# Performance work log

Hardware: AMD Instinct MI355X
Metric: run time of the kernel (lower is better)

The kernel has to match this reference:

```python
import jax, jax.numpy as jnp
import numpy as np

MUL = 256            # multiplicity of each irrep block
S = MUL              # scalar (0e) block width
V = MUL * 3          # vector (1e) block width
D = S + V            # total feature width = 1024
N = 32768            # number of nodes
INV3 = 1.0 / np.sqrt(3.0)   # w3j(1,1,0) and w3j(0,1,1) coefficient
INV6 = 1.0 / np.sqrt(6.0)   # w3j(1,1,1) (Levi-Civita) coefficient
A0 = np.sqrt(1.0 / 5.0)     # path weight for 0e outputs: sqrt(dim_out / n_paths) = sqrt(1/5)
A1 = np.sqrt(3.0 / 5.0)     # path weight for 1e outputs: sqrt(3/5)


def _split(x):
    # x: [N, D] -> scalars [N, MUL], vectors [N, MUL, 3]
    return x[:, :S], x[:, S:].reshape(x.shape[0], MUL, 3)


def norm_gate(x, w1, b1, w2, b2):
    # NormGate: gates = MLP([scalars, |vectors|]); out = [gates_s, vectors * gates_v]
    s, v = _split(x)
    nv = jnp.sqrt(jnp.sum(v * v, axis=-1) + 1e-12)           # [N, MUL] per-irrep norms
    f0 = jnp.concatenate([s, nv], axis=-1)                    # [N, 2*MUL]
    g = jax.nn.silu(f0 @ w1 + b1) @ w2 + b2                   # [N, 2*MUL]
    gated = v * g[:, S:, None]                                # ElementwiseTensorProduct with 0e gates
    return jnp.concatenate([g[:, :S], gated.reshape(-1, V)], axis=-1)


def irrep_linear(x, w0, b0, w1):
    # e3nn o3.Linear: per-l multiplicity mixing with 1/sqrt(fan_in) normalization; bias only on 0e
    s, v = _split(x)
    so = s @ (w0 / np.sqrt(MUL)) + b0
    vo = jnp.einsum('nui,uw->nwi', v, w1 / np.sqrt(MUL))
    return jnp.concatenate([so, vo.reshape(-1, V)], axis=-1)


def tensor_product(x1, x2, w):
    # 'uuu' CG tensor product, 5 instructions: (0,0)->0, (0,1)->1, (1,0)->1, (1,1)->0, (1,1)->1
    # w: [5, MUL] per-path per-u learned weights
    s1, v1 = _split(x1)
    s2, v2 = _split(x2)
    out0 = A0 * (w[0] * s1 * s2 + w[3] * INV3 * jnp.sum(v1 * v2, axis=-1))   # [N, MUL]
    out1 = A1 * (INV3 * (w[1] * s1)[:, :, None] * v2
                 + INV3 * (w[2] * s2)[:, :, None] * v1
                 + INV6 * w[4][None, :, None] * jnp.cross(v1, v2))           # [N, MUL, 3]
    return jnp.concatenate([out0, out1.reshape(-1, V)], axis=-1)


def setup_inputs() -> dict:
    key = jax.random.key(0)
    ks = jax.random.split(key, 32)
    d = {}
    d['x'] = jax.random.normal(ks[0], (N, D), dtype=jnp.float32)
    d['old_fii'] = jax.random.normal(ks[1], (N, D), dtype=jnp.float32)
    i = 2
    for pre in ('ng1', 'ng2', 'ngo'):
        d[pre + '_w1'] = jax.random.normal(ks[i], (2 * MUL, 2 * MUL), dtype=jnp.float32) / np.sqrt(2 * MUL); i += 1
        d[pre + '_b1'] = jax.random.normal(ks[i], (2 * MUL,), dtype=jnp.float32) * 0.01; i += 1
        d[pre + '_w2'] = jax.random.normal(ks[i], (2 * MUL, 2 * MUL), dtype=jnp.float32) / np.sqrt(2 * MUL); i += 1
        d[pre + '_b2'] = jax.random.normal(ks[i], (2 * MUL,), dtype=jnp.float32) * 0.01; i += 1
    for pre in ('lin1', 'lin2', 'lin3'):
        d[pre + '_w0'] = jax.random.normal(ks[i], (MUL, MUL), dtype=jnp.float32); i += 1
        d[pre + '_b0'] = jax.random.normal(ks[i], (MUL,), dtype=jnp.float32) * 0.01; i += 1
        d[pre + '_w1'] = jax.random.normal(ks[i], (MUL, MUL), dtype=jnp.float32); i += 1
    d['tp_w'] = jax.random.normal(ks[i], (5, MUL), dtype=jnp.float32)
    return d


def reference(x, old_fii,
              ng1_w1, ng1_b1, ng1_w2, ng1_b2,
              ng2_w1, ng2_b1, ng2_w2, ng2_b2,
              ngo_w1, ngo_b1, ngo_w2, ngo_b2,
              lin1_w0, lin1_b0, lin1_w1,
              lin2_w0, lin2_b0, lin2_w1,
              lin3_w0, lin3_b0, lin3_w1,
              tp_w):
    xl = irrep_linear(norm_gate(x, ng1_w1, ng1_b1, ng1_w2, ng1_b2), lin1_w0, lin1_b0, lin1_w1)
    xr = irrep_linear(norm_gate(x, ng2_w1, ng2_b1, ng2_w2, ng2_b2), lin2_w0, lin2_b0, lin2_w1)
    t = tensor_product(xl, xr, tp_w) + x        # resnet (dims match)
    t = irrep_linear(norm_gate(t, ngo_w1, ngo_b1, ngo_w2, ngo_b2), lin3_w0, lin3_b0, lin3_w1)
    return old_fii + t
```

## Files before the change

### kernel.cpp

```cpp
#include <hip/hip_runtime.h>
#include <stdint.h>
#include <math.h>

typedef unsigned short u16;
typedef __attribute__((ext_vector_type(8))) short short8;
typedef __attribute__((ext_vector_type(4))) float f32x4;

#define A0C 0.44721359549995793f
#define A1C 0.77459666924148340f
#define INV3C 0.57735026918962584f
#define INV6C 0.40824829046386302f

__device__ __forceinline__ float bf2f(u16 u) {
    unsigned v = ((unsigned)u) << 16; float f; __builtin_memcpy(&f, &v, 4); return f;
}
__device__ __forceinline__ u16 f2bf(float f) {
    unsigned u; __builtin_memcpy(&u, &f, 4);
    u += 0x7fffu + ((u >> 16) & 1u);
    return (u16)(u >> 16);
}

__device__ __forceinline__ void gload_lds16(const void* g, void* l) {
    __builtin_amdgcn_global_load_lds((const __attribute__((address_space(1))) unsigned*)g,
                                     (__attribute__((address_space(3))) unsigned*)l, 16, 0, 0);
}

union S8 { short8 v; u16 h[8]; };

struct WDesc { const float* s; u16* d; int n; float sc; };
struct WArgs { WDesc w[12]; };

__global__ void cvt_weights(WArgs args) {
    WDesc wd = args.w[blockIdx.z];
    int n = wd.n;
    int x0 = blockIdx.x * 32, y0 = blockIdx.y * 32;
    if (x0 >= n || y0 >= n) return;
    __shared__ float tile[32][33];
    int tx = threadIdx.x, ty = threadIdx.y;
#pragma unroll
    for (int j = 0; j < 4; j++)
        tile[ty + 8 * j][tx] = wd.s[(size_t)(y0 + ty + 8 * j) * n + x0 + tx];
    __syncthreads();
#pragma unroll
    for (int j = 0; j < 4; j++)
        wd.d[(size_t)(x0 + ty + 8 * j) * n + y0 + tx] = f2bf(tile[tx][ty + 8 * j] * wd.sc);
}

struct BDesc { const float* s; float* d; int n; };
struct BArgs { BDesc b[9]; };
__global__ void pack_bias(BArgs a) {
    BDesc b = a.b[blockIdx.x];
    for (int i = threadIdx.x; i < b.n; i += 256) b.d[i] = b.s[i];
}

__global__ void prep_f0(const float* __restrict__ x, u16* __restrict__ f0,
                        u16* __restrict__ xv, long ps) {
    int t = blockIdx.x * 256 + threadIdx.x;
    long n = t >> 5;
    int u0 = (t & 31) * 8;
    const float* xr = x + (size_t)n * 1024;
    float4 s0 = *(const float4*)(xr + u0);
    float4 s1 = *(const float4*)(xr + u0 + 4);
    float vv[24];
#pragma unroll
    for (int i = 0; i < 6; i++) {
        float4 w = *(const float4*)(xr + 256 + 3 * u0 + 4 * i);
        vv[4 * i] = w.x; vv[4 * i + 1] = w.y; vv[4 * i + 2] = w.z; vv[4 * i + 3] = w.w;
    }
    float sc[8] = { s0.x, s0.y, s0.z, s0.w, s1.x, s1.y, s1.z, s1.w };
    S8 fs, fn, px, py, pz;
#pragma unroll
    for (int j = 0; j < 8; j++) {
        float a = vv[3 * j], b = vv[3 * j + 1], c = vv[3 * j + 2];
        float nv = sqrtf(a * a + b * b + c * c + 1e-12f);
        fs.h[j] = f2bf(sc[j]);
        fn.h[j] = f2bf(nv);
        px.h[j] = f2bf(a); py.h[j] = f2bf(b); pz.h[j] = f2bf(c);
    }
    size_t o = (size_t)n * 256 + u0;
    *(short8*)(f0 + (size_t)n * 512 + u0) = fs.v;
    *(short8*)(f0 + (size_t)n * 512 + 256 + u0) = fn.v;
    *(short8*)(xv + o) = px.v;
    *(short8*)(xv + ps + o) = py.v;
    *(short8*)(xv + 2 * ps + o) = pz.v;
}

__global__ __launch_bounds__(512, 2)
void gemm256(const u16* __restrict__ Ap, int lda, long az,
             const u16* __restrict__ xsrc,
             const u16* __restrict__ gp, int gld, long gz,
             const u16* __restrict__ Bt, long bz, long bw,
             const float* __restrict__ bias, int bsz,
             u16* __restrict__ C, int ldc, long czs, long czp,
             int K, long nc, int mode, int act, int nshift)
{
    extern __shared__ __align__(16) u16 sm[];
    u16* As = sm;
    u16* Bs = sm + 32768;

    const int tid = threadIdx.x;
    const int lane = tid & 63;
    const int wid = tid >> 6;
    const int wr = wid >> 2, wc = wid & 3;
    const int lr = lane & 15, hk = lane >> 4;

    int nwg = gridDim.x;
    int lid = blockIdx.x;
    int wg;
    if ((nwg & 7) == 0) { int q = nwg >> 3; wg = (lid & 7) * q + (lid >> 3); }
    else wg = lid;
    const long row0 = (long)(wg >> nshift) * 256;
    const int n0 = (wg & ((1 << nshift) - 1)) * 256;
    const int zi = blockIdx.y;

    long p = 0, rr0 = row0;
    if (mode == 2) { p = row0 / nc; rr0 = row0 - p * nc; }

    const u16* Bz = Bt + (size_t)zi * bz + ((mode == 2 && p > 0) ? bw : 0);
    const long cbase = (mode == 2) ? (zi * czs + p * czp + rr0 * ldc)
                                   : (zi * czs + row0 * ldc);

    f32x4 acc[8][4];
#pragma unroll
    for (int m = 0; m < 8; m++)
#pragma unroll
        for (int n = 0; n < 4; n++) acc[m][n] = (f32x4){0.f, 0.f, 0.f, 0.f};

    auto stageB = [&](int buf, int kt) {
#pragma unroll
        for (int it = 0; it < 4; ++it) {
            int idx = it * 512 + tid;
            int r = idx >> 3, s = idx & 7;
            const u16* g = Bz + (size_t)(n0 + r) * K + kt + ((s ^ (r & 7)) * 8);
            u16* l = Bs + buf * 16384 + (size_t)(it * 512 + (tid & 0x1C0)) * 8;
            gload_lds16(g, l);
        }
    };
    auto stageA0 = [&](int buf, int kt) {
#pragma unroll
        for (int it = 0; it < 4; ++it) {
            int idx = it * 512 + tid;
            int r = idx >> 3, s = idx & 7;
            const u16* g = Ap + (size_t)zi * az + (rr0 + r) * (size_t)lda + kt + ((s ^ (r & 7)) * 8);
            u16* l = As + buf * 16384 + (size_t)(it * 512 + (tid & 0x1C0)) * 8;
            gload_lds16(g, l);
        }
    };
    auto stageA2 = [&](int buf, int kt) {
#pragma unroll
        for (int it = 0; it < 4; ++it) {
            int idx = it * 512 + tid;
            int r = idx >> 3, s = idx & 7;
            int u = kt + s * 8;
            S8 gg, tu, pk;
            gg.v = *(const short8*)(gp + (size_t)zi * gz + (rr0 + r) * (size_t)gld + 256 + u);
            tu.v = *(const short8*)(xsrc + (size_t)(row0 - nc + r) * 256 + u);
#pragma unroll
            for (int j = 0; j < 8; j++) pk.h[j] = f2bf(bf2f(tu.h[j]) * bf2f(gg.h[j]));
            *(short8*)&As[buf * 16384 + ((size_t)r * 8 + (s ^ (r & 7))) * 8] = pk.v;
        }
    };

    auto compute = [&](int buf) {
        const int ao = buf * 16384, bo = buf * 16384;
#pragma unroll
        for (int kk = 0; kk < 2; ++kk) {
            short8 b[4];
#pragma unroll
            for (int n = 0; n < 4; n++) {
                int cb = wc * 64 + n * 16 + lr;
                int sl = (kk * 4 + hk) ^ (cb & 7);
                b[n] = *(const short8*)&Bs[bo + (size_t)cb * 64 + sl * 8];
            }
#pragma unroll
            for (int m = 0; m < 8; m++) {
                int ra = wr * 128 + m * 16 + lr;
                int sl = (kk * 4 + hk) ^ (ra & 7);
                short8 a = *(const short8*)&As[ao + (size_t)ra * 64 + sl * 8];
#pragma unroll
                for (int n = 0; n < 4; n++)
                    acc[m][n] = __builtin_amdgcn_mfma_f32_16x16x32_bf16(b[n], a, acc[m][n], 0, 0, 0);
            }
        }
    };

    const bool a_direct = (mode == 0) || (p == 0);
    const int nt = K >> 6;
    int buf = 0;

    if (a_direct) {
        stageB(0, 0);
        stageA0(0, 0);
        for (int t = 0; t < nt; ++t) {
            if (t + 1 < nt) {
                int kt = (t + 1) << 6;
                stageB(buf ^ 1, kt);
                stageA0(buf ^ 1, kt);
                asm volatile("s_waitcnt vmcnt(8)" ::: "memory");
            } else {
                asm volatile("s_waitcnt vmcnt(0)" ::: "memory");
            }
            __builtin_amdgcn_s_barrier();
            __builtin_amdgcn_sched_barrier(0);
            compute(buf);
            __builtin_amdgcn_s_barrier();
            buf ^= 1;
        }
    } else {
        stageB(0, 0);
        stageA2(0, 0);
        __syncthreads();
        for (int t = 0; t < nt; ++t) {
            if (t + 1 < nt) {
                int kt = (t + 1) << 6;
                stageB(buf ^ 1, kt);
                stageA2(buf ^ 1, kt);
            }
            compute(buf);
            __syncthreads();
            buf ^= 1;
        }
    }

    const bool use_bias = bias && (mode == 0 || p == 0);
#pragma unroll
    for (int m = 0; m < 8; m++) {
        long rit = wr * 128 + m * 16 + lr;
        u16* crow = C + cbase + rit * (size_t)ldc;
#pragma unroll
        for (int n = 0; n < 4; n++) {
            int col = n0 + wc * 64 + n * 16 + hk * 4;
            float4 bb = use_bias ? *(const float4*)&bias[(size_t)zi * bsz + col]
                                 : (float4){0.f, 0.f, 0.f, 0.f};
            float v0 = acc[m][n][0] + bb.x;
            float v1 = acc[m][n][1] + bb.y;
            float v2 = acc[m][n][2] + bb.z;
            float v3 = acc[m][n][3] + bb.w;
            if (act) {
                v0 = v0 * (1.0f / (1.0f + __expf(-v0)));
                v1 = v1 * (1.0f / (1.0f + __expf(-v1)));
                v2 = v2 * (1.0f / (1.0f + __expf(-v2)));
                v3 = v3 * (1.0f / (1.0f + __expf(-v3)));
            }
            uint2 st;
            st.x = (unsigned)f2bf(v0) | ((unsigned)f2bf(v1) << 16);
            st.y = (unsigned)f2bf(v2) | ((unsigned)f2bf(v3) << 16);
            *(uint2*)(crow + col) = st;
        }
    }
}

__global__ void tp_res(const u16* __restrict__ xl, const u16* xr_,
                       const float* __restrict__ tpw, const u16* __restrict__ xv,
                       u16* f0, u16* tv, long ps)
{
    int t = blockIdx.x * 256 + threadIdx.x;
    long n = t >> 5;
    int u0 = (t & 31) * 8;
    size_t o = (size_t)n * 256 + u0;

    S8 S1, AX, AY, AZ, S2, BX, BY, BZ, XS, RX, RY, RZ;
    S1.v = *(const short8*)(xl + o);
    AX.v = *(const short8*)(xl + ps + o);
    AY.v = *(const short8*)(xl + 2 * ps + o);
    AZ.v = *(const short8*)(xl + 3 * ps + o);
    S2.v = *(const short8*)(xr_ + o);
    BX.v = *(const short8*)(xr_ + ps + o);
    BY.v = *(const short8*)(xr_ + 2 * ps + o);
    BZ.v = *(const short8*)(xr_ + 3 * ps + o);
    XS.v = *(const short8*)(f0 + (size_t)n * 512 + u0);
    RX.v = *(const short8*)(xv + o);
    RY.v = *(const short8*)(xv + ps + o);
    RZ.v = *(const short8*)(xv + 2 * ps + o);

    float W[5][8];
#pragma unroll
    for (int q = 0; q < 5; q++) {
        float4 a = *(const float4*)(tpw + q * 256 + u0);
        float4 b = *(const float4*)(tpw + q * 256 + u0 + 4);
        W[q][0] = a.x; W[q][1] = a.y; W[q][2] = a.z; W[q][3] = a.w;
        W[q][4] = b.x; W[q][5] = b.y; W[q][6] = b.z; W[q][7] = b.w;
    }

    S8 O0, NV, TX, TY, TZ;
#pragma unroll
    for (int j = 0; j < 8; j++) {
        float s1 = bf2f(S1.h[j]), a1x = bf2f(AX.h[j]), a1y = bf2f(AY.h[j]), a1z = bf2f(AZ.h[j]);
        float s2 = bf2f(S2.h[j]), b1x = bf2f(BX.h[j]), b1y = bf2f(BY.h[j]), b1z = bf2f(BZ.h[j]);
        float dot = a1x * b1x + a1y * b1y + a1z * b1z;
        float cx = a1y * b1z - a1z * b1y;
        float cy = a1z * b1x - a1x * b1z;
        float cz = a1x * b1y - a1y * b1x;
        float out0 = A0C * (W[0][j] * s1 * s2 + W[3][j] * INV3C * dot) + bf2f(XS.h[j]);
        float ox = A1C * (INV3C * (W[1][j] * s1 * b1x + W[2][j] * s2 * a1x) + INV6C * W[4][j] * cx) + bf2f(RX.h[j]);
        float oy = A1C * (INV3C * (W[1][j] * s1 * b1y + W[2][j] * s2 * a1y) + INV6C * W[4][j] * cy) + bf2f(RY.h[j]);
        float oz = A1C * (INV3C * (W[1][j] * s1 * b1z + W[2][j] * s2 * a1z) + INV6C * W[4][j] * cz) + bf2f(RZ.h[j]);
        float nv = sqrtf(ox * ox + oy * oy + oz * oz + 1e-12f);
        O0.h[j] = f2bf(out0);
        NV.h[j] = f2bf(nv);
        TX.h[j] = f2bf(ox); TY.h[j] = f2bf(oy); TZ.h[j] = f2bf(oz);
    }
    *(short8*)(f0 + (size_t)n * 512 + u0) = O0.v;
    *(short8*)(f0 + (size_t)n * 512 + 256 + u0) = NV.v;
    *(short8*)(tv + o) = TX.v;
    *(short8*)(tv + ps + o) = TY.v;
    *(short8*)(tv + 2 * ps + o) = TZ.v;
}

__global__ void repack(const u16* __restrict__ outp, const float* __restrict__ old,
                       float* __restrict__ out, long ps)
{
    int t = blockIdx.x * 256 + threadIdx.x;
    long n = t >> 5;
    int u0 = (t & 31) * 8;
    size_t o = (size_t)n * 256 + u0;

    S8 S, VX, VY, VZ;
    S.v  = *(const short8*)(outp + o);
    VX.v = *(const short8*)(outp + ps + o);
    VY.v = *(const short8*)(outp + 2 * ps + o);
    VZ.v = *(const short8*)(outp + 3 * ps + o);

    const float* oldr = old + (size_t)n * 1024;
    float* outr = out + (size_t)n * 1024;

#pragma unroll
    for (int i = 0; i < 2; i++) {
        float4 ov = *(const float4*)(oldr + u0 + 4 * i);
        float4 r;
        r.x = ov.x + bf2f(S.h[4 * i]);
        r.y = ov.y + bf2f(S.h[4 * i + 1]);
        r.z = ov.z + bf2f(S.h[4 * i + 2]);
        r.w = ov.w + bf2f(S.h[4 * i + 3]);
        *(float4*)(outr + u0 + 4 * i) = r;
    }
    float vv[24];
#pragma unroll
    for (int j = 0; j < 8; j++) {
        vv[3 * j] = bf2f(VX.h[j]);
        vv[3 * j + 1] = bf2f(VY.h[j]);
        vv[3 * j + 2] = bf2f(VZ.h[j]);
    }
#pragma unroll
    for (int i = 0; i < 6; i++) {
        float4 ov = *(const float4*)(oldr + 256 + 3 * u0 + 4 * i);
        float4 r;
        r.x = ov.x + vv[4 * i];
        r.y = ov.y + vv[4 * i + 1];
        r.z = ov.z + vv[4 * i + 2];
        r.w = ov.w + vv[4 * i + 3];
        *(float4*)(outr + 256 + 3 * u0 + 4 * i) = r;
    }
}

enum {
    OFF_ng12w1 = 0,
    OFF_ng1w2  = 524288,
    OFF_ngow1  = 1048576,
    OFF_ngow2  = 1310720,
    OFF_l12w0  = 1572864,
    OFF_l12w1  = 1703936,
    OFF_l3w0   = 1835008,
    OFF_l3w1   = 1900544
};
#define BIAS_BYTE_OFF 3932160
enum { BOFF_mlp1 = 0, BOFF_mlp2 = 1024, BOFF_ngo1 = 2048, BOFF_ngo2 = 2560,
       BOFF_l12 = 3072, BOFF_l3 = 3584 };

extern "C" void kernel_launch(void* const* d_in, const int* in_sizes, int n_in,
                              void* d_out, int out_size, void* d_ws, size_t ws_size,
                              hipStream_t stream) {
    const float* x      = (const float*)d_in[0];
    const float* oldf   = (const float*)d_in[1];
    const float* ng1_w1 = (const float*)d_in[2];
    const float* ng1_b1 = (const float*)d_in[3];
    const float* ng1_w2 = (const float*)d_in[4];
    const float* ng1_b2 = (const float*)d_in[5];
    const float* ng2_w1 = (const float*)d_in[6];
    const float* ng2_b1 = (const float*)d_in[7];
    const float* ng2_w2 = (const float*)d_in[8];
    const float* ng2_b2 = (const float*)d_in[9];
    const float* ngo_w1 = (const float*)d_in[10];
    const float* ngo_b1 = (const float*)d_in[11];
    const float* ngo_w2 = (const float*)d_in[12];
    const float* ngo_b2 = (const float*)d_in[13];
    const float* l1_w0  = (const float*)d_in[14];
    const float* l1_b0  = (const float*)d_in[15];
    const float* l1_w1  = (const float*)d_in[16];
    const float* l2_w0  = (const float*)d_in[17];
    const float* l2_b0  = (const float*)d_in[18];
    const float* l2_w1  = (const float*)d_in[19];
    const float* l3_w0  = (const float*)d_in[20];
    const float* l3_b0  = (const float*)d_in[21];
    const float* l3_w1  = (const float*)d_in[22];
    const float* tpw    = (const float*)d_in[23];

    u16* wts = (u16*)d_ws;
    char* wsb = (char*)d_ws;
    float* biasf = (float*)(wsb + BIAS_BYTE_OFF);

    WArgs wa;
    wa.w[0]  = { ng1_w1, wts + OFF_ng12w1,          512, 1.0f };
    wa.w[1]  = { ng2_w1, wts + OFF_ng12w1 + 262144, 512, 1.0f };
    wa.w[2]  = { ng1_w2, wts + OFF_ng1w2,           512, 1.0f };
    wa.w[3]  = { ng2_w2, wts + OFF_ng1w2 + 262144,  512, 1.0f };
    wa.w[4]  = { ngo_w1, wts + OFF_ngow1,           512, 1.0f };
    wa.w[5]  = { ngo_w2, wts + OFF_ngow2,           512, 1.0f };
    wa.w[6]  = { l1_w0, wts + OFF_l12w0,            256, 0.0625f };
    wa.w[7]  = { l2_w0, wts + OFF_l12w0 + 65536,    256, 0.0625f };
    wa.w[8]  = { l1_w1, wts + OFF_l12w1,            256, 0.0625f };
    wa.w[9]  = { l2_w1, wts + OFF_l12w1 + 65536,    256, 0.0625f };
    wa.w[10] = { l3_w0, wts + OFF_l3w0,             256, 0.0625f };
    wa.w[11] = { l3_w1, wts + OFF_l3w1,             256, 0.0625f };
    cvt_weights<<<dim3(16, 16, 12), dim3(32, 8), 0, stream>>>(wa);

    BArgs ba;
    ba.b[0] = { ng1_b1, biasf + BOFF_mlp1,       512 };
    ba.b[1] = { ng2_b1, biasf + BOFF_mlp1 + 512, 512 };
    ba.b[2] = { ng1_b2, biasf + BOFF_mlp2,       512 };
    ba.b[3] = { ng2_b2, biasf + BOFF_mlp2 + 512, 512 };
    ba.b[4] = { ngo_b1, biasf + BOFF_ngo1,       512 };
    ba.b[5] = { ngo_b2, biasf + BOFF_ngo2,       512 };
    ba.b[6] = { l1_b0, biasf + BOFF_l12,         256 };
    ba.b[7] = { l2_b0, biasf + BOFF_l12 + 256,   256 };
    ba.b[8] = { l3_b0, biasf + BOFF_l3,          256 };
    pack_bias<<<9, 256, 0, stream>>>(ba);

    long Nn = (long)in_sizes[0] / 1024;

    int c = 1;
    while (c < 256 &&
           (unsigned long long)(4ULL << 20) + (unsigned long long)(Nn / c) * 10752ULL > (unsigned long long)ws_size)
        c <<= 1;
    long Nc = Nn / c;

    u16* F0 = (u16*)(wsb + (4 << 20));
    u16* H  = F0 + (size_t)Nc * 512;
    u16* G  = H + (size_t)Nc * 1024;
    u16* XV = G + (size_t)Nc * 1024;
    u16* XL = XV + (size_t)Nc * 768;
    long ps = Nc * 256;
    u16* XR = XL + 4 * ps;
    u16* TV = XR + ps;
    u16* OUTP = XL;

    dim3 blk(512);
    const size_t SMEM = 131072;
    int mt = (int)(Nc / 256);
    int eb = (int)(Nc / 8);

    for (int ch = 0; ch < c; ++ch) {
        const float* xk  = x + (size_t)ch * Nc * 1024;
        const float* ok  = oldf + (size_t)ch * Nc * 1024;
        float* outk = (float*)d_out + (size_t)ch * Nc * 1024;

        prep_f0<<<eb, 256, 0, stream>>>(xk, F0, XV, ps);

        gemm256<<<dim3(mt * 4, 1), blk, SMEM, stream>>>(F0, 512, 0, nullptr, nullptr, 0, 0,
            wts + OFF_ng12w1, 0, 0, biasf + BOFF_mlp1, 0, H, 1024, 0, 0, 512, Nc, 0, 1, 2);
        gemm256<<<dim3(mt * 2, 2), blk, SMEM, stream>>>(H, 1024, 512, nullptr, nullptr, 0, 0,
            wts + OFF_ng1w2, 262144, 0, biasf + BOFF_mlp2, 512, G, 1024, 512, 0, 512, Nc, 0, 0, 1);
        gemm256<<<dim3(mt * 4, 2), blk, SMEM, stream>>>(G, 1024, 512, XV, G, 1024, 512,
            wts + OFF_l12w0, 65536, 131072, biasf + BOFF_l12, 256, XL, 256, 4 * ps, ps, 256, Nc, 2, 0, 0);

        tp_res<<<eb, 256, 0, stream>>>(XL, XR, tpw, XV, F0, TV, ps);

        gemm256<<<dim3(mt * 2, 1), blk, SMEM, stream>>>(F0, 512, 0, nullptr, nullptr, 0, 0,
            wts + OFF_ngow1, 0, 0, biasf + BOFF_ngo1, 0, H, 512, 0, 0, 512, Nc, 0, 1, 1);
        gemm256<<<dim3(mt * 2, 1), blk, SMEM, stream>>>(H, 512, 0, nullptr, nullptr, 0, 0,
            wts + OFF_ngow2, 0, 0, biasf + BOFF_ngo2, 0, G, 512, 0, 0, 512, Nc, 0, 0, 1);
        gemm256<<<dim3(mt * 4, 1), blk, SMEM, stream>>>(G, 512, 0, TV, G, 512, 0,
            wts + OFF_l3w0, 0, 65536, biasf + BOFF_l3, 0, OUTP, 256, 0, ps, 256, Nc, 2, 0, 0);

        repack<<<eb, 256, 0, stream>>>(OUTP, ok, outk, ps);
    }
}
```

Measured before the change: 504.6 us.

## Fuse the two norm-gate MLP GEMMs into one kernel keeping hidden activations in LDS

Adds a mlp_fused kernel that computes silu(F0@W1+b1) for a 64-row tile, keeps the 64x512 hidden tile in shared memory, then multiplies by W2 and writes the gates directly. This replaces two gemm256 launches per MLP, so the hidden matrix H no longer makes a round trip through global memory. The cost is much smaller row tiles (64 rows instead of 256), so weights are re-streamed more often. It also uses 144 KB of LDS per block, which may limit occupancy to one workgroup per CU.

```diff
diff --git a/kernel.cpp b/kernel.cpp
--- a/kernel.cpp
+++ b/kernel.cpp
@@ -83,6 +83,179 @@
     *(short8*)(xv + o) = px.v;
     *(short8*)(xv + ps + o) = py.v;
     *(short8*)(xv + 2 * ps + o) = pz.v;
+}
+
+__global__ __launch_bounds__(512, 2)
+void mlp_fused(const u16* __restrict__ F0, int ldf,
+               const u16* __restrict__ W1, long w1zs,
+               const u16* __restrict__ W2, long w2zs,
+               const float* __restrict__ B1, int b1zs,
+               const float* __restrict__ B2, int b2zs,
+               u16* __restrict__ G, int ldg, int gzoff,
+               long nc)
+{
+    extern __shared__ __align__(16) u16 sm[];
+    u16* Hs = sm;
+    u16* St = sm + 32768;
+
+    const int tid = threadIdx.x;
+    const int lane = tid & 63;
+    const int wid = tid >> 6;
+    const int lr = lane & 15, hk = lane >> 4;
+
+    int nwg = gridDim.x;
+    int lid = blockIdx.x;
+    int wg;
+    if ((nwg & 7) == 0) { int q = nwg >> 3; wg = (lid & 7) * q + (lid >> 3); }
+    else wg = lid;
+    const long rows0 = (long)wg * 64;
+    const int z = blockIdx.y;
+
+    const u16* W1z = W1 + (size_t)z * w1zs;
+    const u16* W2z = W2 + (size_t)z * w2zs;
+    const float* b1 = B1 + (size_t)z * b1zs;
+    const float* b2 = B2 + (size_t)z * b2zs;
+
+    f32x4 acc[4][2];
+
+    auto stageB = [&](const u16* Bh, int buf, int kt) {
+        u16* Bd = St + buf * 20480;
+#pragma unroll
+        for (int it = 0; it < 4; ++it) {
+            int idx = it * 512 + tid;
+            int r = idx >> 3, s = idx & 7;
+            gload_lds16(Bh + (size_t)r * 512 + kt + ((s ^ (r & 7)) * 8),
+                        Bd + (size_t)(it * 512 + (tid & 0x1C0)) * 8);
+        }
+    };
+    auto stageA = [&](int buf, int kt) {
+        u16* Ad = St + buf * 20480 + 16384;
+        int r = tid >> 3, s = tid & 7;
+        gload_lds16(F0 + (rows0 + r) * (size_t)ldf + kt + ((s ^ (r & 7)) * 8),
+                    Ad + (size_t)(tid & 0x1C0) * 8);
+    };
+
+    auto comp1 = [&](int buf) {
+        const u16* Bd = St + buf * 20480;
+        const u16* Ad = Bd + 16384;
+#pragma unroll
+        for (int kk = 0; kk < 2; ++kk) {
+            short8 b[2];
+#pragma unroll
+            for (int n = 0; n < 2; n++) {
+                int cb = wid * 32 + n * 16 + lr;
+                int sl = (kk * 4 + hk) ^ (cb & 7);
+                b[n] = *(const short8*)&Bd[(size_t)cb * 64 + sl * 8];
+            }
+#pragma unroll
+            for (int m = 0; m < 4; m++) {
+                int ra = m * 16 + lr;
+                int sl = (kk * 4 + hk) ^ (ra & 7);
+                short8 a = *(const short8*)&Ad[(size_t)ra * 64 + sl * 8];
+#pragma unroll
+                for (int n = 0; n < 2; n++)
+                    acc[m][n] = __builtin_amdgcn_mfma_f32_16x16x32_bf16(b[n], a, acc[m][n], 0, 0, 0);
+            }
+        }
+    };
+    auto comp2 = [&](int buf, int kt) {
+        const u16* Bd = St + buf * 20480;
+#pragma unroll
+        for (int kk = 0; kk < 2; ++kk) {
+            short8 b[2];
+#pragma unroll
+            for (int n = 0; n < 2; n++) {
+                int cb = wid * 32 + n * 16 + lr;
+                int sl = (kk * 4 + hk) ^ (cb & 7);
+                b[n] = *(const short8*)&Bd[(size_t)cb * 64 + sl * 8];
+            }
+#pragma unroll
+            for (int m = 0; m < 4; m++) {
+                int ra = m * 16 + lr;
+                int slot = ((kt >> 3) + kk * 4 + hk) ^ (ra & 7);
+                short8 a = *(const short8*)&Hs[(size_t)ra * 512 + slot * 8];
+#pragma unroll
+                for (int n = 0; n < 2; n++)
+                    acc[m][n] = __builtin_amdgcn_mfma_f32_16x16x32_bf16(b[n], a, acc[m][n], 0, 0, 0);
+            }
+        }
+    };
+
+    for (int nh = 0; nh < 2; ++nh) {
+        const u16* Bh = W1z + (size_t)nh * 256 * 512;
+#pragma unroll
+        for (int m = 0; m < 4; m++)
+#pragma unroll
+            for (int n = 0; n < 2; n++) acc[m][n] = (f32x4){0.f, 0.f, 0.f, 0.f};
+        stageB(Bh, 0, 0);
+        stageA(0, 0);
+        __syncthreads();
+        int buf = 0;
+        for (int t = 0; t < 8; ++t) {
+            if (t + 1 < 8) { stageB(Bh, buf ^ 1, (t + 1) << 6); stageA(buf ^ 1, (t + 1) << 6); }
+            comp1(buf);
+            __syncthreads();
+            buf ^= 1;
+        }
+#pragma unroll
+        for (int m = 0; m < 4; m++) {
+            int row = m * 16 + lr;
+#pragma unroll
+            for (int n = 0; n < 2; n++) {
+                int col = nh * 256 + wid * 32 + n * 16 + hk * 4;
+                float4 bb = *(const float4*)&b1[col];
+                float v0 = acc[m][n][0] + bb.x;
+                float v1 = acc[m][n][1] + bb.y;
+                float v2 = acc[m][n][2] + bb.z;
+                float v3 = acc[m][n][3] + bb.w;
+                v0 = v0 * (1.0f / (1.0f + __expf(-v0)));
+                v1 = v1 * (1.0f / (1.0f + __expf(-v1)));
+                v2 = v2 * (1.0f / (1.0f + __expf(-v2)));
+                v3 = v3 * (1.0f / (1.0f + __expf(-v3)));
+                uint2 st;
+                st.x = (unsigned)f2bf(v0) | ((unsigned)f2bf(v1) << 16);
+                st.y = (unsigned)f2bf(v2) | ((unsigned)f2bf(v3) << 16);
+                int slot = (col >> 3) ^ (row & 7);
+                *(uint2*)&Hs[(size_t)row * 512 + slot * 8 + (col & 7)] = st;
+            }
+        }
+        __syncthreads();
+    }
+
+    for (int nh = 0; nh < 2; ++nh) {
+        const u16* Bh = W2z + (size_t)nh * 256 * 512;
+#pragma unroll
+        for (int m = 0; m < 4; m++)
+#pragma unroll
+            for (int n = 0; n < 2; n++) acc[m][n] = (f32x4){0.f, 0.f, 0.f, 0.f};
+        stageB(Bh, 0, 0);
+        __syncthreads();
+        int buf = 0;
+        for (int t = 0; t < 8; ++t) {
+            if (t + 1 < 8) stageB(Bh, buf ^ 1, (t + 1) << 6);
+            comp2(buf, t << 6);
+            __syncthreads();
+            buf ^= 1;
+        }
+#pragma unroll
+        for (int m = 0; m < 4; m++) {
+            int row = m * 16 + lr;
+            u16* grow = G + (rows0 + row) * (size_t)ldg + (size_t)z * gzoff;
+#pragma unroll
+            for (int n = 0; n < 2; n++) {
+                int col = nh * 256 + wid * 32 + n * 16 + hk * 4;
+                float4 bb = *(const float4*)&b2[col];
+                float v0 = acc[m][n][0] + bb.x;
+                float v1 = acc[m][n][1] + bb.y;
+                float v2 = acc[m][n][2] + bb.z;
+                float v3 = acc[m][n][3] + bb.w;
+                uint2 st;
+                st.x = (unsigned)f2bf(v0) | ((unsigned)f2bf(v1) << 16);
+                st.y = (unsigned)f2bf(v2) | ((unsigned)f2bf(v3) << 16);
+                *(uint2*)(grow + col) = st;
+            }
+        }
+    }
 }
 
 __global__ __launch_bounds__(512, 2)
@@ -446,7 +619,9 @@
 
     dim3 blk(512);
     const size_t SMEM = 131072;
+    const size_t SMEM_MLP = 147456;
     int mt = (int)(Nc / 256);
+    int fb = (int)(Nc / 64);
     int eb = (int)(Nc / 8);
 
     for (int ch = 0; ch < c; ++ch) {
@@ -456,19 +631,19 @@
 
         prep_f0<<<eb, 256, 0, stream>>>(xk, F0, XV, ps);
 
-        gemm256<<<dim3(mt * 4, 1), blk, SMEM, stream>>>(F0, 512, 0, nullptr, nullptr, 0, 0,
-            wts + OFF_ng12w1, 0, 0, biasf + BOFF_mlp1, 0, H, 1024, 0, 0, 512, Nc, 0, 1, 2);
-        gemm256<<<dim3(mt * 2, 2), blk, SMEM, stream>>>(H, 1024, 512, nullptr, nullptr, 0, 0,
-            wts + OFF_ng1w2, 262144, 0, biasf + BOFF_mlp2, 512, G, 1024, 512, 0, 512, Nc, 0, 0, 1);
+        mlp_fused<<<dim3(fb, 2), blk, SMEM_MLP, stream>>>(
+            F0, 512, wts + OFF_ng12w1, 262144, wts + OFF_ng1w2, 262144,
+            biasf + BOFF_mlp1, 512, biasf + BOFF_mlp2, 512, G, 1024, 512, Nc);
+
         gemm256<<<dim3(mt * 4, 2), blk, SMEM, stream>>>(G, 1024, 512, XV, G, 1024, 512,
             wts + OFF_l12w0, 65536, 131072, biasf + BOFF_l12, 256, XL, 256, 4 * ps, ps, 256, Nc, 2, 0, 0);
 
         tp_res<<<eb, 256, 0, stream>>>(XL, XR, tpw, XV, F0, TV, ps);
 
-        gemm256<<<dim3(mt * 2, 1), blk, SMEM, stream>>>(F0, 512, 0, nullptr, nullptr, 0, 0,
-            wts + OFF_ngow1, 0, 0, biasf + BOFF_ngo1, 0, H, 512, 0, 0, 512, Nc, 0, 1, 1);
-        gemm256<<<dim3(mt * 2, 1), blk, SMEM, stream>>>(H, 512, 0, nullptr, nullptr, 0, 0,
-            wts + OFF_ngow2, 0, 0, biasf + BOFF_ngo2, 0, G, 512, 0, 0, 512, Nc, 0, 0, 1);
+        mlp_fused<<<dim3(fb, 1), blk, SMEM_MLP, stream>>>(
+            F0, 512, wts + OFF_ngow1, 0, wts + OFF_ngow2, 0,
+            biasf + BOFF_ngo1, 0, biasf + BOFF_ngo2, 0, G, 512, 0, Nc);
+
         gemm256<<<dim3(mt * 4, 1), blk, SMEM, stream>>>(G, 512, 0, TV, G, 512, 0,
             wts + OFF_l3w0, 0, 65536, biasf + BOFF_l3, 0, OUTP, 256, 0, ps, 256, Nc, 2, 0, 0);
 
```

Result: slower. 535.0 us (+6.0%).

## Prefetch gated A operand into registers and fuse scalar residual into final GEMM

Applied to the files above, without the earlier changes.

The mode-2 GEMM path now issues the global loads for the gated vector operand before compute and does the multiply/pack into LDS after compute, so load latency overlaps the MFMA work. The final linear GEMM's scalar block (p==0) writes fp32 output directly with bias plus old_fii added, so repack only handles the vector components. This removes a bf16 round trip and a separate read of the scalar part. The cost is extra registers held across compute for the prefetched data, which may lower occupancy.

```diff
diff --git a/kernel.cpp b/kernel.cpp
--- a/kernel.cpp
+++ b/kernel.cpp
@@ -92,7 +92,8 @@
              const u16* __restrict__ Bt, long bz, long bw,
              const float* __restrict__ bias, int bsz,
              u16* __restrict__ C, int ldc, long czs, long czp,
-             int K, long nc, int mode, int act, int nshift)
+             int K, long nc, int mode, int act, int nshift,
+             const float* __restrict__ oldv, float* __restrict__ fout)
 {
     extern __shared__ __align__(16) u16 sm[];
     u16* As = sm;
@@ -146,17 +147,26 @@
             gload_lds16(g, l);
         }
     };
-    auto stageA2 = [&](int buf, int kt) {
+
+    S8 rg[4], rt[4];
+    auto loadA2 = [&](int kt) {
 #pragma unroll
         for (int it = 0; it < 4; ++it) {
             int idx = it * 512 + tid;
             int r = idx >> 3, s = idx & 7;
             int u = kt + s * 8;
-            S8 gg, tu, pk;
-            gg.v = *(const short8*)(gp + (size_t)zi * gz + (rr0 + r) * (size_t)gld + 256 + u);
-            tu.v = *(const short8*)(xsrc + (size_t)(row0 - nc + r) * 256 + u);
-#pragma unroll
-            for (int j = 0; j < 8; j++) pk.h[j] = f2bf(bf2f(tu.h[j]) * bf2f(gg.h[j]));
+            rg[it].v = *(const short8*)(gp + (size_t)zi * gz + (rr0 + r) * (size_t)gld + 256 + u);
+            rt[it].v = *(const short8*)(xsrc + (size_t)(row0 - nc + r) * 256 + u);
+        }
+    };
+    auto packA2 = [&](int buf) {
+#pragma unroll
+        for (int it = 0; it < 4; ++it) {
+            int idx = it * 512 + tid;
+            int r = idx >> 3, s = idx & 7;
+            S8 pk;
+#pragma unroll
+            for (int j = 0; j < 8; j++) pk.h[j] = f2bf(bf2f(rt[it].h[j]) * bf2f(rg[it].h[j]));
             *(short8*)&As[buf * 16384 + ((size_t)r * 8 + (s ^ (r & 7))) * 8] = pk.v;
         }
     };
@@ -207,21 +217,43 @@
             buf ^= 1;
         }
     } else {
+        loadA2(0);
         stageB(0, 0);
-        stageA2(0, 0);
+        packA2(0);
         __syncthreads();
         for (int t = 0; t < nt; ++t) {
-            if (t + 1 < nt) {
+            const bool more = (t + 1 < nt);
+            if (more) {
                 int kt = (t + 1) << 6;
+                loadA2(kt);
                 stageB(buf ^ 1, kt);
-                stageA2(buf ^ 1, kt);
             }
             compute(buf);
+            if (more) packA2(buf ^ 1);
             __syncthreads();
             buf ^= 1;
         }
     }
 
+    if (mode == 2 && p == 0 && fout) {
+#pragma unroll
+        for (int m = 0; m < 8; m++) {
+            long node = rr0 + wr * 128 + m * 16 + lr;
+#pragma unroll
+            for (int n = 0; n < 4; n++) {
+                int col = n0 + wc * 64 + n * 16 + hk * 4;
+                float4 bb = *(const float4*)&bias[col];
+                float4 ov = *(const float4*)&oldv[node * 1024 + col];
+                float4 r;
+                r.x = acc[m][n][0] + bb.x + ov.x;
+                r.y = acc[m][n][1] + bb.y + ov.y;
+                r.z = acc[m][n][2] + bb.z + ov.z;
+                r.w = acc[m][n][3] + bb.w + ov.w;
+                *(float4*)&fout[node * 1024 + col] = r;
+            }
+        }
+        return;
+    }
     const bool use_bias = bias && (mode == 0 || p == 0);
 #pragma unroll
     for (int m = 0; m < 8; m++) {
@@ -315,8 +347,7 @@
     int u0 = (t & 31) * 8;
     size_t o = (size_t)n * 256 + u0;
 
-    S8 S, VX, VY, VZ;
-    S.v  = *(const short8*)(outp + o);
+    S8 VX, VY, VZ;
     VX.v = *(const short8*)(outp + ps + o);
     VY.v = *(const short8*)(outp + 2 * ps + o);
     VZ.v = *(const short8*)(outp + 3 * ps + o);
@@ -324,16 +355,6 @@
     const float* oldr = old + (size_t)n * 1024;
     float* outr = out + (size_t)n * 1024;
 
-#pragma unroll
-    for (int i = 0; i < 2; i++) {
-        float4 ov = *(const float4*)(oldr + u0 + 4 * i);
-        float4 r;
-        r.x = ov.x + bf2f(S.h[4 * i]);
-        r.y = ov.y + bf2f(S.h[4 * i + 1]);
-        r.z = ov.z + bf2f(S.h[4 * i + 2]);
-        r.w = ov.w + bf2f(S.h[4 * i + 3]);
-        *(float4*)(outr + u0 + 4 * i) = r;
-    }
     float vv[24];
 #pragma unroll
     for (int j = 0; j < 8; j++) {
@@ -457,20 +478,26 @@
         prep_f0<<<eb, 256, 0, stream>>>(xk, F0, XV, ps);
 
         gemm256<<<dim3(mt * 4, 1), blk, SMEM, stream>>>(F0, 512, 0, nullptr, nullptr, 0, 0,
-            wts + OFF_ng12w1, 0, 0, biasf + BOFF_mlp1, 0, H, 1024, 0, 0, 512, Nc, 0, 1, 2);
+            wts + OFF_ng12w1, 0, 0, biasf + BOFF_mlp1, 0, H, 1024, 0, 0, 512, Nc, 0, 1, 2,
+            nullptr, nullptr);
         gemm256<<<dim3(mt * 2, 2), blk, SMEM, stream>>>(H, 1024, 512, nullptr, nullptr, 0, 0,
-            wts + OFF_ng1w2, 262144, 0, biasf + BOFF_mlp2, 512, G, 1024, 512, 0, 512, Nc, 0, 0, 1);
+            wts + OFF_ng1w2, 262144, 0, biasf + BOFF_mlp2, 512, G, 1024, 512, 0, 512, Nc, 0, 0, 1,
+            nullptr, nullptr);
         gemm256<<<dim3(mt * 4, 2), blk, SMEM, stream>>>(G, 1024, 512, XV, G, 1024, 512,
-            wts + OFF_l12w0, 65536, 131072, biasf + BOFF_l12, 256, XL, 256, 4 * ps, ps, 256, Nc, 2, 0, 0);
+            wts + OFF_l12w0, 65536, 131072, biasf + BOFF_l12, 256, XL, 256, 4 * ps, ps, 256, Nc, 2, 0, 0,
+            nullptr, nullptr);
 
         tp_res<<<eb, 256, 0, stream>>>(XL, XR, tpw, XV, F0, TV, ps);
 
         gemm256<<<dim3(mt * 2, 1), blk, SMEM, stream>>>(F0, 512, 0, nullptr, nullptr, 0, 0,
-            wts + OFF_ngow1, 0, 0, biasf + BOFF_ngo1, 0, H, 512, 0, 0, 512, Nc, 0, 1, 1);
+            wts + OFF_ngow1, 0, 0, biasf + BOFF_ngo1, 0, H, 512, 0, 0, 512, Nc, 0, 1, 1,
+            nullptr, nullptr);
         gemm256<<<dim3(mt * 2, 1), blk, SMEM, stream>>>(H, 512, 0, nullptr, nullptr, 0, 0,
-            wts + OFF_ngow2, 0, 0, biasf + BOFF_ngo2, 0, G, 512, 0, 0, 512, Nc, 0, 0, 1);
+            wts + OFF_ngow2, 0, 0, biasf + BOFF_ngo2, 0, G, 512, 0, 0, 512, Nc, 0, 0, 1,
+            nullptr, nullptr);
         gemm256<<<dim3(mt * 4, 1), blk, SMEM, stream>>>(G, 512, 0, TV, G, 512, 0,
-            wts + OFF_l3w0, 0, 65536, biasf + BOFF_l3, 0, OUTP, 256, 0, ps, 256, Nc, 2, 0, 0);
+            wts + OFF_l3w0, 0, 65536, biasf + BOFF_l3, 0, OUTP, 256, 0, ps, 256, Nc, 2, 0, 0,
+            ok, outk);
 
         repack<<<eb, 256, 0, stream>>>(OUTP, ok, outk, ps);
     }
```

Result: slower. 517.5 us (+2.5%).
